# Kernel tuning notes

Measured on AMD Instinct MI355X. Metric: run time of the kernel, lower is better.

## Reference

```python
import jax, jax.numpy as jnp
import numpy as np

B, T, N, D = 16, 1024, 1024, 256   # batch, query len (hp.max_T), key len (hp.max_N), hp.d
WIN = 64                            # hp.attention_win_size
NEG = jnp.float32(-2**32 + 1)       # padding value used by the TF module


def setup_inputs() -> dict:
    key = jax.random.key(0)
    k1, k2, k3, k4 = jax.random.split(key, 4)
    Q = jax.random.normal(k1, (B, T, D), dtype=jnp.float32)
    K = jax.random.normal(k2, (B, N, D), dtype=jnp.float32)
    V = jax.random.normal(k3, (B, N, D), dtype=jnp.float32)
    prev_max_attentions = jax.random.randint(k4, (B,), 0, N - WIN, dtype=jnp.int64)
    return {"Q": Q, "K": K, "V": V, "prev_max_attentions": prev_max_attentions}


def reference(Q, K, V, prev_max_attentions):
    # scaled scores: [B, T, N]
    A = jnp.einsum("btd,bnd->btn", Q, K) * jax.lax.rsqrt(jnp.float32(D))

    # monotonic window mask (mono_attention=True):
    idx = jnp.arange(N)                              # [N]
    prev = prev_max_attentions[:, None]              # [B, 1]
    masks = (idx < prev) | (idx >= prev + WIN)       # [B, N], True = disallowed
    A = jnp.where(masks[:, None, :], NEG, A)         # broadcast over T (== tf.tile)

    A = jax.nn.softmax(A, axis=-1)                   # [B, T, N]
    max_attentions = jnp.argmax(A, axis=-1).astype(jnp.float32)  # [B, T]

    R = jnp.concatenate([jnp.einsum("btn,bnd->btd", A, V), Q], axis=-1)  # [B, T, 2D]
    alignments = jnp.transpose(A, (0, 2, 1))         # [B, N, T]
    return (R, alignments, max_attentions)
```

## Files before the change

### kernel.cpp

```cpp
#include <hip/hip_runtime.h>


#define BB 16
#define TT 1024
#define NN 1024
#define DD 256
#define WIN 64
#define TBLK 16
#define NT 256

#define R_ELEMS   (16u*1024u*512u)
#define ALN_ELEMS (16u*1024u*1024u)

__global__ __launch_bounds__(NT, 4) void attn_v9(
    const float* __restrict__ Q, const float* __restrict__ K,
    const float* __restrict__ V, const int* __restrict__ prev_in,
    float* __restrict__ out)
{
    __shared__ float part[4][TBLK][64];
    __shared__ float p_lds[TBLK][WIN + 4];

    float* Rout   = out;
    float* aligns = out + R_ELEMS;
    float* maxatt = out + R_ELEMS + ALN_ELEMS;

    const int tid  = threadIdx.x;
    const int lane = tid & 63;
    const int w    = __builtin_amdgcn_readfirstlane(tid >> 6);
    const int b    = blockIdx.x >> 6;
    const int t0   = (blockIdx.x & 63) * TBLK;
    const int prev = prev_in[b];

    {
        const float4* Kq = (const float4*)(K + ((size_t)b * NN + prev + lane) * DD + w * 64);
        const float*  Qw = Q + ((size_t)b * TT + t0) * DD + w * 64;

        float acc[TBLK];
        #pragma unroll
        for (int t = 0; t < TBLK; ++t) acc[t] = 0.f;

        #pragma unroll
        for (int c = 0; c < 2; ++c) {
            float4 kreg[8];
            #pragma unroll
            for (int d4 = 0; d4 < 8; ++d4) kreg[d4] = Kq[c * 8 + d4];
            #pragma unroll
            for (int t = 0; t < TBLK; ++t) {
                #pragma unroll
                for (int d4 = 0; d4 < 8; ++d4) {
                    float4 q = ((const float4*)(Qw + t * DD))[c * 8 + d4];
                    acc[t] = fmaf(q.x, kreg[d4].x, fmaf(q.y, kreg[d4].y,
                             fmaf(q.z, kreg[d4].z, fmaf(q.w, kreg[d4].w, acc[t]))));
                }
            }
        }
        #pragma unroll
        for (int t = 0; t < TBLK; ++t) part[w][t][lane] = acc[t];
    }
    __syncthreads();

    float4 strip;
    #pragma unroll
    for (int tt = 0; tt < 4; ++tt) {
        const int t = 4 * w + tt;
        float v = (part[0][t][lane] + part[1][t][lane] +
                   part[2][t][lane] + part[3][t][lane]) * 0.0625f;

        float m = v;
        #pragma unroll
        for (int off = 32; off; off >>= 1) m = fmaxf(m, __shfl_xor(m, off));

        float e = expf(v - m);
        float s = e;
        #pragma unroll
        for (int off = 32; off; off >>= 1) s += __shfl_xor(s, off);

        float pv = e / s;
        p_lds[t][lane] = pv;
        ((float*)&strip)[tt] = pv;

        float av = v; int ai = lane;
        #pragma unroll
        for (int off = 32; off; off >>= 1) {
            float ov = __shfl_xor(av, off);
            int   oi = __shfl_xor(ai, off);
            if (ov > av || (ov == av && oi < ai)) { av = ov; ai = oi; }
        }
        if (lane == 0) maxatt[(size_t)b * TT + t0 + t] = (float)(prev + ai);
    }

    *(float4*)(aligns + ((size_t)b * NN + prev + lane) * TT + t0 + 4 * w) = strip;

    {
        const int chunk = blockIdx.x & 63;
        float4* zbase = (float4*)(aligns + (size_t)b * NN * TT);
        const float4 z = make_float4(0.f, 0.f, 0.f, 0.f);
        #pragma unroll
        for (int r = 0; r < 15; ++r) {
            int idx = chunk * 15 + r;
            int n   = idx < prev ? idx : idx + WIN;
            zbase[(size_t)n * 256 + tid] = z;
        }
    }

    {
        const float* qb = Q + ((size_t)b * TT + t0 + 4 * w) * DD;
        const float4* V4 = (const float4*)(V + ((size_t)b * NN + prev) * DD);
        float4 o[4];
        #pragma unroll
        for (int t = 0; t < 4; ++t) o[t] = make_float4(0.f, 0.f, 0.f, 0.f);

        #pragma unroll 4
        for (int j4 = 0; j4 < WIN / 4; ++j4) {
            float4 p0 = *(const float4*)&p_lds[4 * w + 0][j4 * 4];
            float4 p1 = *(const float4*)&p_lds[4 * w + 1][j4 * 4];
            float4 p2 = *(const float4*)&p_lds[4 * w + 2][j4 * 4];
            float4 p3 = *(const float4*)&p_lds[4 * w + 3][j4 * 4];
            float4 v0 = V4[(size_t)(j4 * 4 + 0) * 64 + lane];
            float4 v1 = V4[(size_t)(j4 * 4 + 1) * 64 + lane];
            float4 v2 = V4[(size_t)(j4 * 4 + 2) * 64 + lane];
            float4 v3 = V4[(size_t)(j4 * 4 + 3) * 64 + lane];
            #define ACC4(o_, p_) \
                o_.x = fmaf(p_.x, v0.x, fmaf(p_.y, v1.x, fmaf(p_.z, v2.x, fmaf(p_.w, v3.x, o_.x)))); \
                o_.y = fmaf(p_.x, v0.y, fmaf(p_.y, v1.y, fmaf(p_.z, v2.y, fmaf(p_.w, v3.y, o_.y)))); \
                o_.z = fmaf(p_.x, v0.z, fmaf(p_.y, v1.z, fmaf(p_.z, v2.z, fmaf(p_.w, v3.z, o_.z)))); \
                o_.w = fmaf(p_.x, v0.w, fmaf(p_.y, v1.w, fmaf(p_.z, v2.w, fmaf(p_.w, v3.w, o_.w))));
            ACC4(o[0], p0) ACC4(o[1], p1) ACC4(o[2], p2) ACC4(o[3], p3)
            #undef ACC4
        }

        #pragma unroll
        for (int t = 0; t < 4; ++t) {
            float* Rrow = Rout + ((size_t)b * TT + t0 + 4 * w + t) * (2 * DD);
            ((float4*)Rrow)[lane] = o[t];
            ((float4*)(Rrow + DD))[lane] = ((const float4*)(qb + t * DD))[lane];
        }
    }
}

extern "C" void kernel_launch(void* const* d_in, const int* in_sizes, int n_in,
                              void* d_out, int out_size, void* d_ws, size_t ws_size,
                              hipStream_t stream) {
    const float* Q = (const float*)d_in[0];
    const float* K = (const float*)d_in[1];
    const float* V = (const float*)d_in[2];
    const int* prev = (const int*)d_in[3];
    float* out = (float*)d_out;

    attn_v9<<<BB * TT / TBLK, NT, 0, stream>>>(Q, K, V, prev, out);
}
```

Baseline: 174.9 us.

## Stage K window in LDS and compute full-depth scores per wave

```diff
diff --git a/kernel.cpp b/kernel.cpp
--- a/kernel.cpp
+++ b/kernel.cpp
@@ -6,18 +6,20 @@
 #define NN 1024
 #define DD 256
 #define WIN 64
-#define TBLK 16
-#define NT 256
+#define TBLK 32
+#define NT 512
 
 #define R_ELEMS   (16u*1024u*512u)
 #define ALN_ELEMS (16u*1024u*1024u)
 
-__global__ __launch_bounds__(NT, 4) void attn_v9(
+#define LSTR 260
+
+__global__ __launch_bounds__(NT, 4) void attn_v10(
     const float* __restrict__ Q, const float* __restrict__ K,
     const float* __restrict__ V, const int* __restrict__ prev_in,
     float* __restrict__ out)
 {
-    __shared__ float part[4][TBLK][64];
+    __shared__ float ks[WIN * LSTR];
     __shared__ float p_lds[TBLK][WIN + 4];
 
     float* Rout   = out;
@@ -27,44 +29,40 @@
     const int tid  = threadIdx.x;
     const int lane = tid & 63;
     const int w    = __builtin_amdgcn_readfirstlane(tid >> 6);
-    const int b    = blockIdx.x >> 6;
-    const int t0   = (blockIdx.x & 63) * TBLK;
+    const int b    = blockIdx.x >> 5;
+    const int t0   = (blockIdx.x & 31) * TBLK;
     const int prev = prev_in[b];
 
+    const float* qb = Q + ((size_t)b * TT + t0 + 4 * w) * DD;
+
     {
-        const float4* Kq = (const float4*)(K + ((size_t)b * NN + prev + lane) * DD + w * 64);
-        const float*  Qw = Q + ((size_t)b * TT + t0) * DD + w * 64;
-
-        float acc[TBLK];
+        const float4* Ksrc = (const float4*)(K + ((size_t)b * NN + prev) * DD);
         #pragma unroll
-        for (int t = 0; t < TBLK; ++t) acc[t] = 0.f;
-
-        #pragma unroll
-        for (int c = 0; c < 2; ++c) {
-            float4 kreg[8];
-            #pragma unroll
-            for (int d4 = 0; d4 < 8; ++d4) kreg[d4] = Kq[c * 8 + d4];
-            #pragma unroll
-            for (int t = 0; t < TBLK; ++t) {
-                #pragma unroll
-                for (int d4 = 0; d4 < 8; ++d4) {
-                    float4 q = ((const float4*)(Qw + t * DD))[c * 8 + d4];
-                    acc[t] = fmaf(q.x, kreg[d4].x, fmaf(q.y, kreg[d4].y,
-                             fmaf(q.z, kreg[d4].z, fmaf(q.w, kreg[d4].w, acc[t]))));
-                }
-            }
+        for (int k = 0; k < 8; ++k) {
+            int t4 = tid + k * NT;
+            int r = t4 >> 6, c = t4 & 63;
+            float4 v = Ksrc[(size_t)r * 64 + c];
+            *(float4*)&ks[r * LSTR + c * 4] = v;
         }
-        #pragma unroll
-        for (int t = 0; t < TBLK; ++t) part[w][t][lane] = acc[t];
     }
     __syncthreads();
+
+    float acc[4] = {0.f, 0.f, 0.f, 0.f};
+    #pragma unroll 8
+    for (int d4 = 0; d4 < 64; ++d4) {
+        float4 kk = *(const float4*)&ks[lane * LSTR + d4 * 4];
+        #pragma unroll
+        for (int t = 0; t < 4; ++t) {
+            float4 q = ((const float4*)(qb + t * DD))[d4];
+            acc[t] = fmaf(q.x, kk.x, fmaf(q.y, kk.y, fmaf(q.z, kk.z, fmaf(q.w, kk.w, acc[t]))));
+        }
+    }
 
     float4 strip;
     #pragma unroll
     for (int tt = 0; tt < 4; ++tt) {
         const int t = 4 * w + tt;
-        float v = (part[0][t][lane] + part[1][t][lane] +
-                   part[2][t][lane] + part[3][t][lane]) * 0.0625f;
+        float v = acc[tt] * 0.0625f;
 
         float m = v;
         #pragma unroll
@@ -92,19 +90,18 @@
     *(float4*)(aligns + ((size_t)b * NN + prev + lane) * TT + t0 + 4 * w) = strip;
 
     {
-        const int chunk = blockIdx.x & 63;
+        const int chunk = blockIdx.x & 31;
         float4* zbase = (float4*)(aligns + (size_t)b * NN * TT);
         const float4 z = make_float4(0.f, 0.f, 0.f, 0.f);
         #pragma unroll
         for (int r = 0; r < 15; ++r) {
-            int idx = chunk * 15 + r;
+            int idx = chunk * 30 + 2 * r + (tid >> 8);
             int n   = idx < prev ? idx : idx + WIN;
-            zbase[(size_t)n * 256 + tid] = z;
+            zbase[(size_t)n * 256 + (tid & 255)] = z;
         }
     }
 
     {
-        const float* qb = Q + ((size_t)b * TT + t0 + 4 * w) * DD;
         const float4* V4 = (const float4*)(V + ((size_t)b * NN + prev) * DD);
         float4 o[4];
         #pragma unroll
@@ -147,5 +144,5 @@
     const int* prev = (const int*)d_in[3];
     float* out = (float*)d_out;
 
-    attn_v9<<<BB * TT / TBLK, NT, 0, stream>>>(Q, K, V, prev, out);
+    attn_v10<<<BB * TT / TBLK, NT, 0, stream>>>(Q, K, V, prev, out);
 }
```

New measurement: 174.5 us. No clear change (-0.2%).
